# Kernel optimization log

Measured on AMD Instinct MI355X. Metric: run time of the kernel, lower is better.

The kernel has to match this reference:

```python
import jax, jax.numpy as jnp
import numpy as np

N = 100000      # nodes
E = 3200000     # edges (before self-loops)
F_IN = 512      # input feature dim
HEADS = 8
DIM = 8         # per-head dim for hidden layers
HID = HEADS * DIM  # 64
CLS = 40        # num_classes
NEG_SLOPE = 0.2 # PyG GATConv default leaky relu slope


def setup_inputs() -> dict:
    key = jax.random.key(0)
    ks = jax.random.split(key, 14)
    def glorot(k, shape, fan_in):
        return jax.random.normal(k, shape, jnp.float32) * (1.0 / np.sqrt(fan_in))
    return {
        "x": jax.random.normal(ks[0], (N, F_IN), jnp.float32),
        "edge_index": jax.random.randint(ks[1], (2, E), 0, N, dtype=jnp.int32),
        # layer 1: in=F_IN, heads=8, dim=8, concat
        "W1": glorot(ks[2], (F_IN, HEADS * DIM), F_IN),
        "a_src1": glorot(ks[3], (HEADS, DIM), DIM),
        "a_dst1": glorot(ks[4], (HEADS, DIM), DIM),
        "b1": jnp.zeros((HEADS * DIM,), jnp.float32),
        # layer 2: in=64, heads=8, dim=8, concat
        "W2": glorot(ks[5], (HID, HEADS * DIM), HID),
        "a_src2": glorot(ks[6], (HEADS, DIM), DIM),
        "a_dst2": glorot(ks[7], (HEADS, DIM), DIM),
        "b2": jnp.zeros((HEADS * DIM,), jnp.float32),
        # layer 3: in=64, heads=1, dim=CLS, no concat (mean over heads == identity)
        "W3": glorot(ks[8], (HID, CLS), HID),
        "a_src3": glorot(ks[9], (1, CLS), CLS),
        "a_dst3": glorot(ks[10], (1, CLS), CLS),
        "b3": jnp.zeros((CLS,), jnp.float32),
    }


def gat_layer(h_in, W, att_src, att_dst, bias, src, dst, heads, dim, concat):
    # h_in: [N, F], W: [F, heads*dim], att_*: [heads, dim]
    n = h_in.shape[0]
    h = (h_in @ W).reshape(n, heads, dim)                    # [N, H, D]
    a_s = jnp.sum(h * att_src, axis=-1)                      # [N, H]
    a_d = jnp.sum(h * att_dst, axis=-1)                      # [N, H]
    e = jax.nn.leaky_relu(a_s[src] + a_d[dst], NEG_SLOPE)    # [E', H] edge logits
    # segment-softmax over incoming edges of each dst node (self-loops guarantee non-empty)
    m = jax.ops.segment_max(e, dst, num_segments=n)          # [N, H]
    p = jnp.exp(e - m[dst])
    s = jax.ops.segment_sum(p, dst, num_segments=n)          # [N, H]
    alpha = p / s[dst]                                       # [E', H]
    out = jax.ops.segment_sum(alpha[:, :, None] * h[src], dst, num_segments=n)  # [N, H, D]
    out = out.reshape(n, heads * dim) if concat else out.mean(axis=1)
    return out + bias


def reference(x, edge_index, W1, a_src1, a_dst1, b1, W2, a_src2, a_dst2, b2, W3, a_src3, a_dst3, b3):
    # PyG GATConv default add_self_loops=True
    loops = jnp.arange(N, dtype=edge_index.dtype)
    src = jnp.concatenate([edge_index[0], loops])
    dst = jnp.concatenate([edge_index[1], loops])
    h = gat_layer(x, W1, a_src1, a_dst1, b1, src, dst, HEADS, DIM, True)
    h = jax.nn.elu(h)  # dropout inactive in eval mode
    h = gat_layer(h, W2, a_src2, a_dst2, b2, src, dst, HEADS, DIM, True)
    h = jax.nn.elu(h)
    h = gat_layer(h, W3, a_src3, a_dst3, b3, src, dst, 1, CLS, False)
    return jax.nn.log_softmax(h, axis=1)
```

## Files before the change

kernel.cpp:

```cpp
#include <hip/hip_runtime.h>
#include <math.h>

#define NN 100000
#define EE 3200000
#define ET 3300000
#define FIN 512
#define HDIM 64
#define NCLS 40

#define NBUK 512
#define NPB 196
#define NBUK_USED 511
#define EPB 4096
#define EPT 16
#define CAP 8192

typedef __attribute__((ext_vector_type(8))) short frag_ab;
typedef __attribute__((ext_vector_type(4))) float frag_cd;

#define CVTPK(dst, a, b) asm("v_cvt_pk_bf16_f32 %0, %1, %2" : "=v"(dst) : "v"(a), "v"(b))

__device__ inline unsigned short f2bf(float f){
  union { float f; unsigned int u; } x; x.f = f;
  unsigned int u = x.u;
  unsigned int r = u + 0x7FFF + ((u >> 16) & 1);
  return (unsigned short)(r >> 16);
}
__device__ inline float bflo(unsigned u){
  union { unsigned u; float f; } x; x.u = u << 16; return x.f;
}
__device__ inline float bfhi(unsigned u){
  union { unsigned u; float f; } x; x.u = u & 0xFFFF0000u; return x.f;
}
__device__ inline float bf2f(unsigned short u){
  union { unsigned int u; float f; } x; x.u = ((unsigned int)u) << 16;
  return x.f;
}
__device__ inline unsigned fkey(float f){
  union { float f; unsigned u; } x; x.f = f;
  return (x.u >> 31) ? ~x.u : (x.u | 0x80000000u);
}
__device__ inline float funkey(unsigned k){
  union { unsigned u; float f; } x;
  x.u = (k & 0x80000000u) ? (k ^ 0x80000000u) : ~k;
  return x.f;
}

__global__ void k_prep(const float* __restrict__ W1, const float* __restrict__ W2, const float* __restrict__ W3,
                       const float* __restrict__ as1, const float* __restrict__ ad1,
                       const float* __restrict__ as2, const float* __restrict__ ad2,
                       const float* __restrict__ as3, const float* __restrict__ ad3,
                       unsigned short* __restrict__ Wt1, unsigned short* __restrict__ Wt2,
                       unsigned short* __restrict__ Wt3, float* __restrict__ attv,
                       int* __restrict__ bcur, unsigned* __restrict__ gmax){
  int i = blockIdx.x*256 + threadIdx.x;
  if(i < NBUK) bcur[i] = 0;
  if(i < 32) gmax[i] = 0u;
  if(i < 32768){
    int n = i >> 9, k = i & 511;
    Wt1[i] = f2bf(W1[k*HDIM + n]);
  } else if(i < 36864){
    int i2 = i - 32768; int n = i2 >> 6, k = i2 & 63;
    Wt2[i2] = f2bf(W2[k*HDIM + n]);
  } else if(i < 40960){
    int i3 = i - 36864; int n = i3 >> 6, k = i3 & 63;
    Wt3[i3] = (n < NCLS) ? f2bf(W3[k*NCLS + n]) : (unsigned short)0;
  } else if(i < 41312){
    int j = i - 40960;
    const float L2E = 1.4426950408889634f;
    float v;
    if(j < 64) v = as1[j]*L2E;
    else if(j < 128) v = ad1[j-64]*L2E;
    else if(j < 192) v = as2[j-128]*L2E;
    else if(j < 256) v = ad2[j-192]*L2E;
    else if(j < 304){ int q=j-256; v = (q<NCLS)? as3[q]*L2E : 0.f; }
    else { int q=j-304; v = (q<NCLS)? ad3[q]*L2E : 0.f; }
    attv[j] = v;
  }
}

__global__ __launch_bounds__(256) void k_bucket(const int* __restrict__ src, const int* __restrict__ dst,
                                                int* __restrict__ bcur, int* __restrict__ pbuf){
  __shared__ int lcnt[NBUK];
  __shared__ int lbase[NBUK];
  int t = threadIdx.x;
  for(int i=t;i<NBUK;i+=256) lcnt[i]=0;
  __syncthreads();
  int base = blockIdx.x*EPB + t;
  int bk[EPT], rk[EPT], pk[EPT];
  #pragma unroll
  for(int j=0;j<EPT;j++){
    int e = base + j*256;
    bk[j] = -1;
    if(e < ET){
      int s, d;
      if(e < EE){ s = src[e]; d = dst[e]; } else { s = e - EE; d = s; }
      int b = d / NPB;
      bk[j] = b;
      pk[j] = s | ((d - b*NPB) << 17);
      rk[j] = atomicAdd(&lcnt[b], 1);
    }
  }
  __syncthreads();
  for(int i=t;i<NBUK;i+=256){
    int v = lcnt[i];
    lbase[i] = v ? atomicAdd(&bcur[i], v) : 0;
  }
  __syncthreads();
  #pragma unroll
  for(int j=0;j<EPT;j++){
    if(bk[j] >= 0){
      int pos = lbase[bk[j]] + rk[j];
      if(pos < CAP) pbuf[(size_t)bk[j]*CAP + pos] = pk[j];
    }
  }
}

__global__ __launch_bounds__(256) void k_bfinal(const int* __restrict__ bcur, const int* __restrict__ pbuf,
                                                int* __restrict__ rp, int* __restrict__ col){
  __shared__ int red[256];
  __shared__ int cnt[NPB];
  int b = blockIdx.x, t = threadIdx.x;
  int part = 0;
  for(int i=t; i<b; i+=256) part += bcur[i];
  red[t] = part;
  __syncthreads();
  for(int off=128; off; off>>=1){
    if(t < off) red[t] += red[t+off];
    __syncthreads();
  }
  int beg = red[0];
  int cntb = bcur[b];
  const int* pb = pbuf + (size_t)b*CAP;
  for(int i=t;i<NPB;i+=256) cnt[i]=0;
  __syncthreads();
  for(int i=t; i<cntb; i+=256){
    int dloc = pb[i] >> 17;
    atomicAdd(&cnt[dloc], 1);
  }
  __syncthreads();
  if(t < 64){
    int vals[4]; int sum = 0;
    #pragma unroll
    for(int j=0;j<4;j++){ int idx = t*4+j; int v = (idx<NPB)?cnt[idx]:0; vals[j]=v; sum+=v; }
    int incl = sum;
    #pragma unroll
    for(int off=1; off<64; off<<=1){
      int x = __shfl_up(incl, off);
      if(t >= off) incl += x;
    }
    int run = incl - sum;
    #pragma unroll
    for(int j=0;j<4;j++){
      int idx = t*4+j;
      if(idx < NPB){ int v = vals[j]; cnt[idx] = run; run += v; }
    }
  }
  __syncthreads();
  int node0 = b*NPB;
  int nloc = NN - node0; if(nloc > NPB) nloc = NPB;
  for(int i=t;i<nloc;i+=256){
    int g = beg + cnt[i];
    rp[node0 + i] = g;
    cnt[i] = g;
  }
  if(b == 0 && t == 0) rp[NN] = ET;
  __syncthreads();
  for(int i=t; i<cntb; i+=256){
    int v = pb[i];
    int s = v & 0x1FFFF;
    int dloc = v >> 17;
    int pos = atomicAdd(&cnt[dloc], 1);
    col[pos] = s;
  }
}

template<int CT>
__device__ inline void att_epi8(const frag_cd (&acc)[2][CT], int rowbase, int fr, int kg,
                                const float* __restrict__ asv, const float* __restrict__ adv,
                                unsigned short* __restrict__ as_o, float* __restrict__ ad_o,
                                float (*gml)[8], int w, int M){
  float av[CT], dv[CT];
  #pragma unroll
  for(int j=0;j<CT;j++){ av[j]=asv[j*16+fr]; dv[j]=adv[j*16+fr]; }
  float mx[CT];
  #pragma unroll
  for(int j=0;j<CT;j++) mx[j] = -1e38f;
  #pragma unroll
  for(int i=0;i<2;i++){
    #pragma unroll
    for(int r=0;r<4;r++){
      int row = rowbase + i*16 + kg*4 + r;
      float ps[CT], pd[CT];
      #pragma unroll
      for(int j=0;j<CT;j++){ float v = acc[i][j][r]; ps[j]=v*av[j]; pd[j]=v*dv[j]; }
      #pragma unroll
      for(int mk=1; mk<8; mk<<=1){
        #pragma unroll
        for(int j=0;j<CT;j++){ ps[j]+=__shfl_xor(ps[j],mk); pd[j]+=__shfl_xor(pd[j],mk); }
      }
      if((fr&7)==0 && row < M){
        int half = fr>>3;
        uint2 s2;
        CVTPK(s2.x, ps[0], ps[1]);
        CVTPK(s2.y, ps[2], ps[3]);
        *(uint2*)&as_o[row*8 + half*4] = s2;
        float4 d4; d4.x=pd[0]; d4.y=pd[1]; d4.z=pd[2]; d4.w=pd[3];
        *(float4*)&ad_o[row*8 + half*4] = d4;
        #pragma unroll
        for(int j=0;j<CT;j++) mx[j] = fmaxf(mx[j], ps[j]);
      }
    }
  }
  #pragma unroll
  for(int j=0;j<CT;j++){
    mx[j] = fmaxf(mx[j], __shfl_xor(mx[j],16));
    mx[j] = fmaxf(mx[j], __shfl_xor(mx[j],32));
  }
  if(kg==0 && (fr&7)==0){
    int half = fr>>3;
    #pragma unroll
    for(int j=0;j<CT;j++) gml[w][half*4 + j] = mx[j];
  }
}

template<int CT>
__device__ inline void att_epi1(const frag_cd (&acc)[2][CT], int rowbase, int fr, int kg,
                                const float* __restrict__ asv, const float* __restrict__ adv,
                                float* __restrict__ as_o, float* __restrict__ ad_o,
                                float (*gml)[8], int w, int lane, int M){
  float av[CT], dv[CT];
  #pragma unroll
  for(int j=0;j<CT;j++){ av[j]=asv[j*16+fr]; dv[j]=adv[j*16+fr]; }
  float mx = -1e38f;
  #pragma unroll
  for(int i=0;i<2;i++){
    #pragma unroll
    for(int r=0;r<4;r++){
      int row = rowbase + i*16 + kg*4 + r;
      float ps=0.f, pd=0.f;
      #pragma unroll
      for(int j=0;j<CT;j++){ float v = acc[i][j][r]; ps += v*av[j]; pd += v*dv[j]; }
      #pragma unroll
      for(int mk=1; mk<16; mk<<=1){ ps+=__shfl_xor(ps,mk); pd+=__shfl_xor(pd,mk); }
      if(row < M){
        mx = fmaxf(mx, ps);
        if(fr==0){ as_o[row]=ps; ad_o[row]=pd; }
      }
    }
  }
  #pragma unroll
  for(int mk=1; mk<64; mk<<=1) mx = fmaxf(mx, __shfl_xor(mx, mk));
  if(lane==0) gml[w][0] = mx;
}

#define BM 128
#define BK 32
#define LSTR 40
__global__ __launch_bounds__(256) void k_gemm1(const float* __restrict__ A, const unsigned short* __restrict__ Wt,
                                               const float* __restrict__ asv, const float* __restrict__ adv,
                                               unsigned short* __restrict__ Out,
                                               unsigned short* __restrict__ as_o, float* __restrict__ ad_o,
                                               unsigned* __restrict__ gmax, int M){
  __shared__ __attribute__((aligned(16))) unsigned short Al[2][BM*LSTR];
  __shared__ __attribute__((aligned(16))) unsigned short Bl[2][64*LSTR];
  __shared__ float gml[4][8];
  int t = threadIdx.x;
  int w = t >> 6, l = t & 63;
  int row0 = blockIdx.x * BM;

  int srow = t >> 1;
  int shalf = t & 1;
  int bn = t >> 2;
  int bseg = t & 3;

  int fr = l & 15, kg = l >> 4;

  frag_cd acc[2][4];
  #pragma unroll
  for(int i=0;i<2;i++)
    #pragma unroll
    for(int j=0;j<4;j++) acc[i][j] = (frag_cd){0.f,0.f,0.f,0.f};

  int rg = row0 + srow; if(rg >= M) rg = M-1;
  const float* aprow = &A[(size_t)rg*FIN + shalf*16];

  #define STAGE(buf, kc) do { \
    const float* ap = aprow + (kc); \
    float4 v0 = *(const float4*)(ap); \
    float4 v1 = *(const float4*)(ap+4); \
    float4 v2 = *(const float4*)(ap+8); \
    float4 v3 = *(const float4*)(ap+12); \
    uint4 pa, pb; \
    CVTPK(pa.x, v0.x, v0.y); CVTPK(pa.y, v0.z, v0.w); \
    CVTPK(pa.z, v1.x, v1.y); CVTPK(pa.w, v1.z, v1.w); \
    CVTPK(pb.x, v2.x, v2.y); CVTPK(pb.y, v2.z, v2.w); \
    CVTPK(pb.z, v3.x, v3.y); CVTPK(pb.w, v3.z, v3.w); \
    *(uint4*)&Al[buf][srow*LSTR + shalf*16] = pa; \
    *(uint4*)&Al[buf][srow*LSTR + shalf*16 + 8] = pb; \
    *(uint4*)&Bl[buf][bn*LSTR + bseg*8] = *(const uint4*)&Wt[bn*FIN + (kc) + bseg*8]; \
  } while(0)

  STAGE(0, 0);
  __syncthreads();

  #pragma unroll 1
  for(int step = 0; step < FIN/BK; ++step){
    int buf = step & 1;
    if(step + 1 < FIN/BK) STAGE(buf^1, (step+1)*BK);
    frag_ab af[2], bfr[4];
    #pragma unroll
    for(int i=0;i<2;i++) af[i] = *(const frag_ab*)&Al[buf][(w*32 + i*16 + fr)*LSTR + kg*8];
    #pragma unroll
    for(int j=0;j<4;j++) bfr[j] = *(const frag_ab*)&Bl[buf][(j*16 + fr)*LSTR + kg*8];
    #pragma unroll
    for(int i=0;i<2;i++)
      #pragma unroll
      for(int j=0;j<4;j++)
        acc[i][j] = __builtin_amdgcn_mfma_f32_16x16x32_bf16(af[i], bfr[j], acc[i][j], 0, 0, 0);
    __syncthreads();
  }

  #pragma unroll
  for(int i=0;i<2;i++){
    int crow = row0 + w*32 + i*16 + kg*4;
    #pragma unroll
    for(int j=0;j<4;j++){
      int ccol = j*16 + fr;
      #pragma unroll
      for(int r=0;r<4;r++){
        if(crow + r < M) Out[(size_t)(crow+r)*HDIM + ccol] = f2bf(acc[i][j][r]);
      }
    }
  }
  att_epi8(acc, row0 + w*32, fr, kg, asv, adv, as_o, ad_o, gml, w, M);
  __syncthreads();
  if(t < 8){
    float v = fmaxf(fmaxf(gml[0][t], gml[1][t]), fmaxf(gml[2][t], gml[3][t]));
    atomicMax(&gmax[t], fkey(v));
  }
  #undef STAGE
}

template<int K, int C, int HEADS>
__global__ __launch_bounds__(256) void k_gemmb(const unsigned short* __restrict__ A,
                                               const unsigned short* __restrict__ Wt,
                                               const float* __restrict__ asv, const float* __restrict__ adv,
                                               unsigned short* __restrict__ Out,
                                               void* __restrict__ as_o, float* __restrict__ ad_o,
                                               unsigned* __restrict__ gmax, int M){
  constexpr int CT = (C + 15)/16;
  __shared__ __attribute__((aligned(16))) unsigned short Al[2][BM*LSTR];
  __shared__ __attribute__((aligned(16))) unsigned short Bl[2][64*LSTR];
  __shared__ float gml[4][8];
  int t = threadIdx.x;
  int w = t >> 6, l = t & 63;
  int row0 = blockIdx.x * BM;

  int srow = t >> 1;
  int shalf = t & 1;
  int bn = t >> 2;
  int bseg = t & 3;

  int fr = l & 15, kg = l >> 4;

  frag_cd acc[2][CT];
  #pragma unroll
  for(int i=0;i<2;i++)
    #pragma unroll
    for(int j=0;j<CT;j++) acc[i][j] = (frag_cd){0.f,0.f,0.f,0.f};

  int rg = row0 + srow; if(rg >= M) rg = M-1;
  const unsigned short* aprow = &A[(size_t)rg*K + shalf*16];

  #define STAGEB(buf, kc) do { \
    *(uint4*)&Al[buf][srow*LSTR + shalf*16]     = *(const uint4*)(aprow + (kc)); \
    *(uint4*)&Al[buf][srow*LSTR + shalf*16 + 8] = *(const uint4*)(aprow + (kc) + 8); \
    *(uint4*)&Bl[buf][bn*LSTR + bseg*8] = *(const uint4*)&Wt[bn*K + (kc) + bseg*8]; \
  } while(0)

  STAGEB(0, 0);
  __syncthreads();

  #pragma unroll 1
  for(int step = 0; step < K/BK; ++step){
    int buf = step & 1;
    if(step + 1 < K/BK) STAGEB(buf^1, (step+1)*BK);
    frag_ab af[2], bfr[CT];
    #pragma unroll
    for(int i=0;i<2;i++) af[i] = *(const frag_ab*)&Al[buf][(w*32 + i*16 + fr)*LSTR + kg*8];
    #pragma unroll
    for(int j=0;j<CT;j++) bfr[j] = *(const frag_ab*)&Bl[buf][(j*16 + fr)*LSTR + kg*8];
    #pragma unroll
    for(int i=0;i<2;i++)
      #pragma unroll
      for(int j=0;j<CT;j++)
        acc[i][j] = __builtin_amdgcn_mfma_f32_16x16x32_bf16(af[i], bfr[j], acc[i][j], 0, 0, 0);
    __syncthreads();
  }

  #pragma unroll
  for(int i=0;i<2;i++){
    int crow = row0 + w*32 + i*16 + kg*4;
    #pragma unroll
    for(int j=0;j<CT;j++){
      int ccol = j*16 + fr;
      if(ccol >= C) continue;
      #pragma unroll
      for(int r=0;r<4;r++){
        if(crow + r < M) Out[(size_t)(crow+r)*C + ccol] = f2bf(acc[i][j][r]);
      }
    }
  }
  if(HEADS == 8){
    att_epi8(acc, row0 + w*32, fr, kg, asv, adv, (unsigned short*)as_o, ad_o, gml, w, M);
    __syncthreads();
    if(t < 8){
      float v = fmaxf(fmaxf(gml[0][t], gml[1][t]), fmaxf(gml[2][t], gml[3][t]));
      atomicMax(&gmax[t], fkey(v));
    }
  } else {
    att_epi1(acc, row0 + w*32, fr, kg, asv, adv, (float*)as_o, ad_o, gml, w, l, M);
    __syncthreads();
    if(t == 0){
      float v = fmaxf(fmaxf(gml[0][0], gml[1][0]), fmaxf(gml[2][0], gml[3][0]));
      atomicMax(&gmax[0], fkey(v));
    }
  }
  #undef STAGEB
}

template<bool DO_ELU>
__global__ __launch_bounds__(256) void k_agg8(const unsigned short* __restrict__ hbf, const int* __restrict__ rp,
                      const int* __restrict__ col,
                      const unsigned short* __restrict__ asb, const float* __restrict__ ad_,
                      const unsigned* __restrict__ gmax,
                      const float* __restrict__ bias, unsigned short* __restrict__ out){
  int gid = blockIdx.x*256 + threadIdx.x;
  int node = gid >> 6, lane = gid & 63;
  if(node >= NN) return;
  int el = lane >> 3;
  int fl = lane & 7;
  int px = ((fl&1)<<2) | (fl>>1);
  int beg = rp[node], end = rp[node+1];
  int deg = end - beg;
  float adn = ad_[node*8 + px];
  float M = funkey(gmax[px]) + adn;
  M = fmaxf(M, 0.2f*M);
  float s = 0.f;
  float a[8] = {0.f,0.f,0.f,0.f,0.f,0.f,0.f,0.f};

  for(int base = 0; base < deg; base += 64){
    int cnt = deg - base; if(cnt > 64) cnt = 64;
    int idx = 0;
    if(lane < cnt) idx = col[beg + base + lane];
    int jf = cnt & ~7;
    int j = 0;
    for(; j < jf; j += 8){
      int sn = __shfl(idx, j + el);
      float ea = bf2f(asb[sn*8 + px]);
      uint4 h = *(const uint4*)&hbf[(size_t)sn*HDIM + fl*8];
      float e = ea + adn; e = fmaxf(e, 0.2f*e);
      float p = exp2f(e - M);
      s += p;
      a[0] = fmaf(p, bflo(h.x), a[0]); a[1] = fmaf(p, bfhi(h.x), a[1]);
      a[2] = fmaf(p, bflo(h.y), a[2]); a[3] = fmaf(p, bfhi(h.y), a[3]);
      a[4] = fmaf(p, bflo(h.z), a[4]); a[5] = fmaf(p, bfhi(h.z), a[5]);
      a[6] = fmaf(p, bflo(h.w), a[6]); a[7] = fmaf(p, bfhi(h.w), a[7]);
    }
    if(j < cnt){
      int sn = __shfl(idx, j + el);
      float ea = bf2f(asb[sn*8 + px]);
      uint4 h = *(const uint4*)&hbf[(size_t)sn*HDIM + fl*8];
      float e = ea + adn; e = fmaxf(e, 0.2f*e);
      float p = (j + el < cnt) ? exp2f(e - M) : 0.f;
      s += p;
      a[0] = fmaf(p, bflo(h.x), a[0]); a[1] = fmaf(p, bfhi(h.x), a[1]);
      a[2] = fmaf(p, bflo(h.y), a[2]); a[3] = fmaf(p, bfhi(h.y), a[3]);
      a[4] = fmaf(p, bflo(h.z), a[4]); a[5] = fmaf(p, bfhi(h.z), a[5]);
      a[6] = fmaf(p, bflo(h.w), a[6]); a[7] = fmaf(p, bfhi(h.w), a[7]);
    }
  }

  #pragma unroll
  for(int wd=8; wd<=32; wd<<=1){
    s += __shfl_xor(s, wd);
    #pragma unroll
    for(int i=0;i<8;i++) a[i] += __shfl_xor(a[i], wd);
  }

  if(el == 0){
    float inv = 1.f/s;
    float4 b0 = *(const float4*)&bias[fl*8];
    float4 b1 = *(const float4*)&bias[fl*8 + 4];
    float o[8];
    o[0]=a[0]*inv+b0.x; o[1]=a[1]*inv+b0.y; o[2]=a[2]*inv+b0.z; o[3]=a[3]*inv+b0.w;
    o[4]=a[4]*inv+b1.x; o[5]=a[5]*inv+b1.y; o[6]=a[6]*inv+b1.z; o[7]=a[7]*inv+b1.w;
    if(DO_ELU){
      #pragma unroll
      for(int i=0;i<8;i++) o[i] = (o[i] > 0.f) ? o[i] : expm1f(o[i]);
    }
    uint4 pk;
    CVTPK(pk.x, o[0], o[1]); CVTPK(pk.y, o[2], o[3]);
    CVTPK(pk.z, o[4], o[5]); CVTPK(pk.w, o[6], o[7]);
    *(uint4*)&out[(size_t)node*HDIM + fl*8] = pk;
  }
}

__global__ __launch_bounds__(256) void k_agg1(const unsigned short* __restrict__ hbf, const int* __restrict__ rp,
                      const int* __restrict__ col,
                      const float* __restrict__ as_, const float* __restrict__ ad_,
                      const unsigned* __restrict__ gmax,
                      const float* __restrict__ bias, float* __restrict__ out){
  int gid = blockIdx.x*256 + threadIdx.x;
  int node = gid >> 6, lane = gid & 63;
  if(node >= NN) return;
  int el = lane >> 3;
  int fl = lane & 7;
  bool act = fl < 5;
  int f0 = act ? fl*8 : 0;
  int beg = rp[node], end = rp[node+1];
  int deg = end - beg;
  float adn = ad_[node];
  float M = funkey(gmax[0]) + adn;
  M = fmaxf(M, 0.2f*M);
  float s = 0.f;
  float a[8] = {0.f,0.f,0.f,0.f,0.f,0.f,0.f,0.f};

  for(int base = 0; base < deg; base += 64){
    int cnt = deg - base; if(cnt > 64) cnt = 64;
    int idx = 0;
    if(lane < cnt) idx = col[beg + base + lane];
    for(int j = 0; j < cnt; j += 8){
      int sn = __shfl(idx, j + el);
      float ea = as_[sn];
      uint4 h = *(const uint4*)&hbf[(size_t)sn*NCLS + f0];
      float e = ea + adn; e = fmaxf(e, 0.2f*e);
      float p = (j + el < cnt) ? exp2f(e - M) : 0.f;
      s += p;
      a[0] = fmaf(p, bflo(h.x), a[0]); a[1] = fmaf(p, bfhi(h.x), a[1]);
      a[2] = fmaf(p, bflo(h.y), a[2]); a[3] = fmaf(p, bfhi(h.y), a[3]);
      a[4] = fmaf(p, bflo(h.z), a[4]); a[5] = fmaf(p, bfhi(h.z), a[5]);
      a[6] = fmaf(p, bflo(h.w), a[6]); a[7] = fmaf(p, bfhi(h.w), a[7]);
    }
  }

  #pragma unroll
  for(int wd=8; wd<=32; wd<<=1){
    s += __shfl_xor(s, wd);
    #pragma unroll
    for(int i=0;i<8;i++) a[i] += __shfl_xor(a[i], wd);
  }

  float inv = 1.f/s;
  float o[8];
  #pragma unroll
  for(int i=0;i<8;i++) o[i] = a[i]*inv + (act ? bias[f0+i] : 0.f);

  float vmax = act ? fmaxf(fmaxf(fmaxf(o[0],o[1]),fmaxf(o[2],o[3])),
                           fmaxf(fmaxf(o[4],o[5]),fmaxf(o[6],o[7]))) : -INFINITY;
  #pragma unroll
  for(int wd=1; wd<8; wd<<=1) vmax = fmaxf(vmax, __shfl_xor(vmax, wd));
  float ex = 0.f;
  if(act){
    #pragma unroll
    for(int i=0;i<8;i++) ex += expf(o[i] - vmax);
  }
  #pragma unroll
  for(int wd=1; wd<8; wd<<=1) ex += __shfl_xor(ex, wd);
  float lg = logf(ex);
  if(el == 0 && act){
    float4 r0, r1;
    r0.x=o[0]-vmax-lg; r0.y=o[1]-vmax-lg; r0.z=o[2]-vmax-lg; r0.w=o[3]-vmax-lg;
    r1.x=o[4]-vmax-lg; r1.y=o[5]-vmax-lg; r1.z=o[6]-vmax-lg; r1.w=o[7]-vmax-lg;
    *(float4*)&out[(size_t)node*NCLS + f0]     = r0;
    *(float4*)&out[(size_t)node*NCLS + f0 + 4] = r1;
  }
}

static inline size_t alignup(size_t x){ return (x + 255) & ~(size_t)255; }

extern "C" void kernel_launch(void* const* d_in, const int* in_sizes, int n_in,
                              void* d_out, int out_size, void* d_ws, size_t ws_size,
                              hipStream_t stream){
  const float* x      = (const float*)d_in[0];
  const int*   ei     = (const int*)d_in[1];
  const float* W1     = (const float*)d_in[2];
  const float* asrc1  = (const float*)d_in[3];
  const float* adst1  = (const float*)d_in[4];
  const float* b1     = (const float*)d_in[5];
  const float* W2     = (const float*)d_in[6];
  const float* asrc2  = (const float*)d_in[7];
  const float* adst2  = (const float*)d_in[8];
  const float* b2     = (const float*)d_in[9];
  const float* W3     = (const float*)d_in[10];
  const float* asrc3  = (const float*)d_in[11];
  const float* adst3  = (const float*)d_in[12];
  const float* b3     = (const float*)d_in[13];
  const int* src = ei;
  const int* dst = ei + EE;

  char* w = (char*)d_ws;
  int* rp     = (int*)w;              w += alignup((size_t)(NN+1)*4);
  int* bcur   = (int*)w;              w += alignup((size_t)NBUK*4);
  unsigned* gmax = (unsigned*)w;      w += alignup(32*4);
  unsigned short* Wt1 = (unsigned short*)w; w += alignup((size_t)64*FIN*2);
  unsigned short* Wt2 = (unsigned short*)w; w += alignup((size_t)64*HDIM*2);
  unsigned short* Wt3 = (unsigned short*)w; w += alignup((size_t)64*HDIM*2);
  float* attv = (float*)w;            w += alignup((size_t)352*4);
  int* col    = (int*)w;              w += alignup((size_t)ET*4);
  int* pbuf   = (int*)w;              w += alignup((size_t)NBUK*CAP*4);
  unsigned short* hAb = (unsigned short*)w; w += alignup((size_t)NN*HDIM*2 + 256);
  unsigned short* hBb = (unsigned short*)w; w += alignup((size_t)NN*HDIM*2 + 256);
  unsigned short* hCb = (unsigned short*)w; w += alignup((size_t)NN*NCLS*2 + 256);
  unsigned short* asb = (unsigned short*)w; w += alignup((size_t)NN*8*2 + 256);
  float* as3  = (float*)w;            w += alignup((size_t)NN*4);
  float* adA  = (float*)w;            w += alignup((size_t)NN*8*4);

  dim3 blk(256);
  int gWav  = (NN*64 + 255)/256;
  int gG1   = (NN + BM - 1)/BM;
  int gBuk  = (ET + EPB - 1)/EPB;

  k_prep<<<(41312 + 255)/256, blk, 0, stream>>>(W1, W2, W3, asrc1, adst1, asrc2, adst2, asrc3, adst3,
                                                Wt1, Wt2, Wt3, attv, bcur, gmax);
  k_bucket<<<gBuk, blk, 0, stream>>>(src, dst, bcur, pbuf);
  k_bfinal<<<NBUK_USED, blk, 0, stream>>>(bcur, pbuf, rp, col);

  k_gemm1<<<gG1, blk, 0, stream>>>(x, Wt1, attv + 0, attv + 64, hAb, asb, adA, gmax + 0, NN);
  k_agg8<true><<<gWav, blk, 0, stream>>>(hAb, rp, col, asb, adA, gmax + 0, b1, hBb);

  k_gemmb<HDIM, HDIM, 8><<<gG1, blk, 0, stream>>>(hBb, Wt2, attv + 128, attv + 192, hAb, asb, adA, gmax + 8, NN);
  k_agg8<true><<<gWav, blk, 0, stream>>>(hAb, rp, col, asb, adA, gmax + 8, b2, hBb);

  k_gemmb<HDIM, NCLS, 1><<<gG1, blk, 0, stream>>>(hBb, Wt3, attv + 256, attv + 304, hCb, as3, adA, gmax + 16, NN);
  k_agg1<<<gWav, blk, 0, stream>>>(hCb, rp, col, as3, adA, gmax + 16, b3, (float*)d_out);
}
```

Before: 401.3 us.

## Co-schedule CSR build blocks with layer-1 GEMM tiles in combined kernels

The edge bucketing and CSR finalize kernels are merged into two launches that also carry half each of the layer-1 GEMM tiles. The aim is for the memory-bound graph preprocessing to overlap with the compute-heavy projection and to remove separate launches. Buffer zeroing moves to a hipMemsetAsync. The layer-3 feature buffer is padded to a 64-element row stride so the aggregation loads stay aligned. The cost is a larger combined kernel whose shared-memory reuse and register pressure may lower occupancy, and a hardcoded tile split.

```diff
diff --git a/kernel.cpp b/kernel.cpp
--- a/kernel.cpp
+++ b/kernel.cpp
@@ -7,6 +7,7 @@
 #define FIN 512
 #define HDIM 64
 #define NCLS 40
+#define OST3 64
 
 #define NBUK 512
 #define NPB 196
@@ -15,6 +16,10 @@
 #define EPT 16
 #define CAP 8192
 
+#define G1TILES 782
+#define G1H 391
+#define GBUK 806
+
 typedef __attribute__((ext_vector_type(8))) short frag_ab;
 typedef __attribute__((ext_vector_type(4))) float frag_cd;
 
@@ -51,11 +56,8 @@
                        const float* __restrict__ as2, const float* __restrict__ ad2,
                        const float* __restrict__ as3, const float* __restrict__ ad3,
                        unsigned short* __restrict__ Wt1, unsigned short* __restrict__ Wt2,
-                       unsigned short* __restrict__ Wt3, float* __restrict__ attv,
-                       int* __restrict__ bcur, unsigned* __restrict__ gmax){
+                       unsigned short* __restrict__ Wt3, float* __restrict__ attv){
   int i = blockIdx.x*256 + threadIdx.x;
-  if(i < NBUK) bcur[i] = 0;
-  if(i < 32) gmax[i] = 0u;
   if(i < 32768){
     int n = i >> 9, k = i & 511;
     Wt1[i] = f2bf(W1[k*HDIM + n]);
@@ -79,102 +81,6 @@
   }
 }
 
-__global__ __launch_bounds__(256) void k_bucket(const int* __restrict__ src, const int* __restrict__ dst,
-                                                int* __restrict__ bcur, int* __restrict__ pbuf){
-  __shared__ int lcnt[NBUK];
-  __shared__ int lbase[NBUK];
-  int t = threadIdx.x;
-  for(int i=t;i<NBUK;i+=256) lcnt[i]=0;
-  __syncthreads();
-  int base = blockIdx.x*EPB + t;
-  int bk[EPT], rk[EPT], pk[EPT];
-  #pragma unroll
-  for(int j=0;j<EPT;j++){
-    int e = base + j*256;
-    bk[j] = -1;
-    if(e < ET){
-      int s, d;
-      if(e < EE){ s = src[e]; d = dst[e]; } else { s = e - EE; d = s; }
-      int b = d / NPB;
-      bk[j] = b;
-      pk[j] = s | ((d - b*NPB) << 17);
-      rk[j] = atomicAdd(&lcnt[b], 1);
-    }
-  }
-  __syncthreads();
-  for(int i=t;i<NBUK;i+=256){
-    int v = lcnt[i];
-    lbase[i] = v ? atomicAdd(&bcur[i], v) : 0;
-  }
-  __syncthreads();
-  #pragma unroll
-  for(int j=0;j<EPT;j++){
-    if(bk[j] >= 0){
-      int pos = lbase[bk[j]] + rk[j];
-      if(pos < CAP) pbuf[(size_t)bk[j]*CAP + pos] = pk[j];
-    }
-  }
-}
-
-__global__ __launch_bounds__(256) void k_bfinal(const int* __restrict__ bcur, const int* __restrict__ pbuf,
-                                                int* __restrict__ rp, int* __restrict__ col){
-  __shared__ int red[256];
-  __shared__ int cnt[NPB];
-  int b = blockIdx.x, t = threadIdx.x;
-  int part = 0;
-  for(int i=t; i<b; i+=256) part += bcur[i];
-  red[t] = part;
-  __syncthreads();
-  for(int off=128; off; off>>=1){
-    if(t < off) red[t] += red[t+off];
-    __syncthreads();
-  }
-  int beg = red[0];
-  int cntb = bcur[b];
-  const int* pb = pbuf + (size_t)b*CAP;
-  for(int i=t;i<NPB;i+=256) cnt[i]=0;
-  __syncthreads();
-  for(int i=t; i<cntb; i+=256){
-    int dloc = pb[i] >> 17;
-    atomicAdd(&cnt[dloc], 1);
-  }
-  __syncthreads();
-  if(t < 64){
-    int vals[4]; int sum = 0;
-    #pragma unroll
-    for(int j=0;j<4;j++){ int idx = t*4+j; int v = (idx<NPB)?cnt[idx]:0; vals[j]=v; sum+=v; }
-    int incl = sum;
-    #pragma unroll
-    for(int off=1; off<64; off<<=1){
-      int x = __shfl_up(incl, off);
-      if(t >= off) incl += x;
-    }
-    int run = incl - sum;
-    #pragma unroll
-    for(int j=0;j<4;j++){
-      int idx = t*4+j;
-      if(idx < NPB){ int v = vals[j]; cnt[idx] = run; run += v; }
-    }
-  }
-  __syncthreads();
-  int node0 = b*NPB;
-  int nloc = NN - node0; if(nloc > NPB) nloc = NPB;
-  for(int i=t;i<nloc;i+=256){
-    int g = beg + cnt[i];
-    rp[node0 + i] = g;
-    cnt[i] = g;
-  }
-  if(b == 0 && t == 0) rp[NN] = ET;
-  __syncthreads();
-  for(int i=t; i<cntb; i+=256){
-    int v = pb[i];
-    int s = v & 0x1FFFF;
-    int dloc = v >> 17;
-    int pos = atomicAdd(&cnt[dloc], 1);
-    col[pos] = s;
-  }
-}
-
 template<int CT>
 __device__ inline void att_epi8(const frag_cd (&acc)[2][CT], int rowbase, int fr, int kg,
                                 const float* __restrict__ asv, const float* __restrict__ adv,
@@ -257,23 +163,124 @@
 #define BM 128
 #define BK 32
 #define LSTR 40
-__global__ __launch_bounds__(256) void k_gemm1(const float* __restrict__ A, const unsigned short* __restrict__ Wt,
-                                               const float* __restrict__ asv, const float* __restrict__ adv,
-                                               unsigned short* __restrict__ Out,
-                                               unsigned short* __restrict__ as_o, float* __restrict__ ad_o,
-                                               unsigned* __restrict__ gmax, int M){
+template<int PHASE>
+__global__ __launch_bounds__(256) void k_mix(const float* __restrict__ A, const unsigned short* __restrict__ Wt,
+                                             const float* __restrict__ asv, const float* __restrict__ adv,
+                                             unsigned short* __restrict__ Out,
+                                             unsigned short* __restrict__ as_o, float* __restrict__ ad_o,
+                                             unsigned* __restrict__ gmax,
+                                             const int* __restrict__ src, const int* __restrict__ dst,
+                                             int* __restrict__ bcur, int* __restrict__ pbuf,
+                                             int* __restrict__ rp, int* __restrict__ col){
   __shared__ __attribute__((aligned(16))) unsigned short Al[2][BM*LSTR];
   __shared__ __attribute__((aligned(16))) unsigned short Bl[2][64*LSTR];
   __shared__ float gml[4][8];
   int t = threadIdx.x;
+
+  if(blockIdx.x >= G1H){
+    int* shi = (int*)&Al[0][0];
+    if(PHASE == 0){
+      int bb = blockIdx.x - G1H;
+      int* lcnt  = shi;
+      int* lbase = shi + NBUK;
+      for(int i=t;i<NBUK;i+=256) lcnt[i]=0;
+      __syncthreads();
+      int base = bb*EPB + t;
+      int bk[EPT], rk[EPT], pk[EPT];
+      #pragma unroll
+      for(int j=0;j<EPT;j++){
+        int e = base + j*256;
+        bk[j] = -1;
+        if(e < ET){
+          int s, d;
+          if(e < EE){ s = src[e]; d = dst[e]; } else { s = e - EE; d = s; }
+          int b = d / NPB;
+          bk[j] = b;
+          pk[j] = s | ((d - b*NPB) << 17);
+          rk[j] = atomicAdd(&lcnt[b], 1);
+        }
+      }
+      __syncthreads();
+      for(int i=t;i<NBUK;i+=256){
+        int v = lcnt[i];
+        lbase[i] = v ? atomicAdd(&bcur[i], v) : 0;
+      }
+      __syncthreads();
+      #pragma unroll
+      for(int j=0;j<EPT;j++){
+        if(bk[j] >= 0){
+          int pos = lbase[bk[j]] + rk[j];
+          if(pos < CAP) pbuf[(size_t)bk[j]*CAP + pos] = pk[j];
+        }
+      }
+    } else {
+      int b = blockIdx.x - G1H;
+      int* red = shi;
+      int* cnt = shi + 256;
+      int part = 0;
+      for(int i=t; i<b; i+=256) part += bcur[i];
+      red[t] = part;
+      __syncthreads();
+      for(int off=128; off; off>>=1){
+        if(t < off) red[t] += red[t+off];
+        __syncthreads();
+      }
+      int beg = red[0];
+      int cntb = bcur[b];
+      const int* pb = pbuf + (size_t)b*CAP;
+      for(int i=t;i<NPB;i+=256) cnt[i]=0;
+      __syncthreads();
+      for(int i=t; i<cntb; i+=256){
+        int dloc = pb[i] >> 17;
+        atomicAdd(&cnt[dloc], 1);
+      }
+      __syncthreads();
+      if(t < 64){
+        int vals[4]; int sum = 0;
+        #pragma unroll
+        for(int j=0;j<4;j++){ int idx = t*4+j; int v = (idx<NPB)?cnt[idx]:0; vals[j]=v; sum+=v; }
+        int incl = sum;
+        #pragma unroll
+        for(int off=1; off<64; off<<=1){
+          int x = __shfl_up(incl, off);
+          if(t >= off) incl += x;
+        }
+        int run = incl - sum;
+        #pragma unroll
+        for(int j=0;j<4;j++){
+          int idx = t*4+j;
+          if(idx < NPB){ int v = vals[j]; cnt[idx] = run; run += v; }
+        }
+      }
+      __syncthreads();
+      int node0 = b*NPB;
+      int nloc = NN - node0; if(nloc > NPB) nloc = NPB;
+      for(int i=t;i<nloc;i+=256){
+        int g = beg + cnt[i];
+        rp[node0 + i] = g;
+        cnt[i] = g;
+      }
+      if(b == 0 && t == 0) rp[NN] = ET;
+      __syncthreads();
+      for(int i=t; i<cntb; i+=256){
+        int v = pb[i];
+        int s = v & 0x1FFFF;
+        int dloc = v >> 17;
+        int pos = atomicAdd(&cnt[dloc], 1);
+        col[pos] = s;
+      }
+    }
+    return;
+  }
+
   int w = t >> 6, l = t & 63;
-  int row0 = blockIdx.x * BM;
+  int row0 = (blockIdx.x + PHASE*G1H) * BM;
+  int M = NN;
 
   int srow = t >> 1;
   int shalf = t & 1;
   int bn = t >> 2;
   int bseg = t & 3;
-
   int fr = l & 15, kg = l >> 4;
 
   frag_cd acc[2][4];
@@ -342,7 +349,7 @@
   #undef STAGE
 }
 
-template<int K, int C, int HEADS>
+template<int K, int C, int OST, int HEADS>
 __global__ __launch_bounds__(256) void k_gemmb(const unsigned short* __restrict__ A,
                                                const unsigned short* __restrict__ Wt,
                                                const float* __restrict__ asv, const float* __restrict__ adv,
@@ -361,7 +368,6 @@
   int shalf = t & 1;
   int bn = t >> 2;
   int bseg = t & 3;
-
   int fr = l & 15, kg = l >> 4;
 
   frag_cd acc[2][CT];
@@ -408,7 +414,7 @@
       if(ccol >= C) continue;
       #pragma unroll
       for(int r=0;r<4;r++){
-        if(crow + r < M) Out[(size_t)(crow+r)*C + ccol] = f2bf(acc[i][j][r]);
+        if(crow + r < M) Out[(size_t)(crow+r)*OST + ccol] = f2bf(acc[i][j][r]);
       }
     }
   }
@@ -534,7 +540,7 @@
     for(int j = 0; j < cnt; j += 8){
       int sn = __shfl(idx, j + el);
       float ea = as_[sn];
-      uint4 h = *(const uint4*)&hbf[(size_t)sn*NCLS + f0];
+      uint4 h = *(const uint4*)&hbf[(size_t)sn*OST3 + f0];
       float e = ea + adn; e = fmaxf(e, 0.2f*e);
       float p = (j + el < cnt) ? exp2f(e - M) : 0.f;
       s += p;
@@ -612,7 +618,7 @@
   int* pbuf   = (int*)w;              w += alignup((size_t)NBUK*CAP*4);
   unsigned short* hAb = (unsigned short*)w; w += alignup((size_t)NN*HDIM*2 + 256);
   unsigned short* hBb = (unsigned short*)w; w += alignup((size_t)NN*HDIM*2 + 256);
-  unsigned short* hCb = (unsigned short*)w; w += alignup((size_t)NN*NCLS*2 + 256);
+  unsigned short* hCb = (unsigned short*)w; w += alignup((size_t)NN*OST3*2 + 256);
   unsigned short* asb = (unsigned short*)w; w += alignup((size_t)NN*8*2 + 256);
   float* as3  = (float*)w;            w += alignup((size_t)NN*4);
   float* adA  = (float*)w;            w += alignup((size_t)NN*8*4);
@@ -620,19 +626,20 @@
   dim3 blk(256);
   int gWav  = (NN*64 + 255)/256;
   int gG1   = (NN + BM - 1)/BM;
-  int gBuk  = (ET + EPB - 1)/EPB;
-
+
+  hipMemsetAsync(bcur, 0, 2048 + 128, stream);
   k_prep<<<(41312 + 255)/256, blk, 0, stream>>>(W1, W2, W3, asrc1, adst1, asrc2, adst2, asrc3, adst3,
-                                                Wt1, Wt2, Wt3, attv, bcur, gmax);
-  k_bucket<<<gBuk, blk, 0, stream>>>(src, dst, bcur, pbuf);
-  k_bfinal<<<NBUK_USED, blk, 0, stream>>>(bcur, pbuf, rp, col);
-
-  k_gemm1<<<gG1, blk, 0, stream>>>(x, Wt1, attv + 0, attv + 64, hAb, asb, adA, gmax + 0, NN);
+                                                Wt1, Wt2, Wt3, attv);
+  k_mix<0><<<G1H + GBUK, blk, 0, stream>>>(x, Wt1, attv + 0, attv + 64, hAb, asb, adA, gmax + 0,
+                                           src, dst, bcur, pbuf, rp, col);
+  k_mix<1><<<G1H + NBUK_USED, blk, 0, stream>>>(x, Wt1, attv + 0, attv + 64, hAb, asb, adA, gmax + 0,
+                                                src, dst, bcur, pbuf, rp, col);
+
   k_agg8<true><<<gWav, blk, 0, stream>>>(hAb, rp, col, asb, adA, gmax + 0, b1, hBb);
 
-  k_gemmb<HDIM, HDIM, 8><<<gG1, blk, 0, stream>>>(hBb, Wt2, attv + 128, attv + 192, hAb, asb, adA, gmax + 8, NN);
+  k_gemmb<HDIM, HDIM, HDIM, 8><<<gG1, blk, 0, stream>>>(hBb, Wt2, attv + 128, attv + 192, hAb, asb, adA, gmax + 8, NN);
   k_agg8<true><<<gWav, blk, 0, stream>>>(hAb, rp, col, asb, adA, gmax + 8, b2, hBb);
 
-  k_gemmb<HDIM, NCLS, 1><<<gG1, blk, 0, stream>>>(hBb, Wt3, attv + 256, attv + 304, hCb, as3, adA, gmax + 16, NN);
+  k_gemmb<HDIM, NCLS, OST3, 1><<<gG1, blk, 0, stream>>>(hBb, Wt3, attv + 256, attv + 304, hCb, as3, adA, gmax + 16, NN);
   k_agg1<<<gWav, blk, 0, stream>>>(hCb, rp, col, as3, adA, gmax + 16, b3, (float*)d_out);
 }
```

After: 390.3 us. -2.7%, faster.
